# Performance work log

Hardware: AMD Instinct MI355X
Metric: run time of the kernel (lower is better)

The kernel has to match this reference:

```python
import jax, jax.numpy as jnp
import numpy as np

N = 100000
D = 128
H = 128
E = 3200000

def setup_inputs() -> dict:
    key = jax.random.key(0)
    ks = jax.random.split(key, 6)
    x = jax.random.normal(ks[0], (N, D), dtype=jnp.float32)
    edge_src = jax.random.randint(ks[1], (E,), 0, N, dtype=jnp.int32)
    edge_dst = jax.random.randint(ks[2], (E,), 0, N, dtype=jnp.int32)
    edge_w = jax.random.uniform(ks[3], (E,), dtype=jnp.float32)
    # Linear params (torch default-ish scale)
    W1 = jax.random.normal(ks[4], (D, H), dtype=jnp.float32) / np.sqrt(D)
    b1 = jnp.zeros((H,), dtype=jnp.float32)
    W2 = jax.random.normal(ks[5], (H, H), dtype=jnp.float32) / np.sqrt(H)
    b2 = jnp.zeros((H,), dtype=jnp.float32)
    return {"x": x, "edge_src": edge_src, "edge_dst": edge_dst, "edge_w": edge_w,
            "W1": W1, "b1": b1, "W2": W2, "b2": b2}

def reference(x, edge_src, edge_dst, edge_w, W1, b1, W2, b2):
    # out = spmm(A, x): weighted aggregation of source-node features at dst
    msgs = x[edge_src] * edge_w[:, None]           # [E, D]
    agg = jax.ops.segment_sum(msgs, edge_dst, num_segments=N)  # [N, D]
    out = agg + x                                   # residual
    out = jax.nn.selu(out @ W1 + b1)                # layer 1
    out = jax.nn.selu(out @ W2 + b2)                # layer 2
    return out
```

## Files before the change

### kernel.cpp

```cpp
#include <hip/hip_runtime.h>
#include <hip/hip_bf16.h>

#define SELU_LAM   1.0507009873554805f
#define SELU_ALPHA 1.6732632423543772f

#define NBSH 6
#define NPB  64
#define RCAP 4096
#define SCHUNK 16384
#define MROWS 64

typedef __attribute__((ext_vector_type(8))) short bf16x8;
typedef __attribute__((ext_vector_type(4))) float f32x4;

__device__ __forceinline__ float selu_f(float v) {
    return v > 0.0f ? SELU_LAM * v
                    : (SELU_LAM * SELU_ALPHA) * (expf(v) - 1.0f);
}

__device__ __forceinline__ unsigned bf16r(float f) {
    unsigned u = __float_as_uint(f);
    return (u + 0x7FFFu + ((u >> 16) & 1u)) >> 16;
}

__global__ __launch_bounds__(256) void prep_kernel(const float* __restrict__ x,
                                                   uint* __restrict__ xb, int nxb,
                                                   const float* __restrict__ W1,
                                                   const float* __restrict__ W2,
                                                   uint* __restrict__ wt1,
                                                   uint* __restrict__ wt2,
                                                   const int* __restrict__ edst,
                                                   int* __restrict__ bcnt, int E, int B) {
    __shared__ int lc[2048];
    for (int i = threadIdx.x; i < B; i += 256) lc[i] = 0;

    int tid = blockIdx.x * 256 + threadIdx.x;
    int stride = gridDim.x * 256;

    for (int i = tid; i < nxb; i += stride) {
        float2 v = ((const float2*)x)[i];
        xb[i] = bf16r(v.x) | (bf16r(v.y) << 16);
    }
    for (int i = tid; i < 128 * 64; i += stride) {
        int n = i & 127, kp = i >> 7;
        uint idx = (uint)(((n * 128 + 2 * kp) ^ ((n & 7) << 3)) >> 1);
        uint lo = bf16r(W1[(2 * kp) * 128 + n]);
        uint hi = bf16r(W1[(2 * kp + 1) * 128 + n]);
        wt1[idx] = lo | (hi << 16);
        lo = bf16r(W2[(2 * kp) * 128 + n]);
        hi = bf16r(W2[(2 * kp + 1) * 128 + n]);
        wt2[idx] = lo | (hi << 16);
    }
    __syncthreads();
    int n4 = E >> 2;
    for (int j = tid; j < n4; j += stride) {
        int4 d = ((const int4*)edst)[j];
        atomicAdd(&lc[d.x >> NBSH], 1);
        atomicAdd(&lc[d.y >> NBSH], 1);
        atomicAdd(&lc[d.z >> NBSH], 1);
        atomicAdd(&lc[d.w >> NBSH], 1);
    }
    for (int j = (n4 << 2) + tid; j < E; j += stride) atomicAdd(&lc[edst[j] >> NBSH], 1);
    __syncthreads();
    for (int i = threadIdx.x; i < B; i += 256) if (lc[i]) atomicAdd(&bcnt[i], lc[i]);
}

__global__ __launch_bounds__(1024) void bucket_scan(const int* __restrict__ bcnt,
                                                    int* __restrict__ boff,
                                                    int* __restrict__ bfill, int B, int E) {
    __shared__ int buf[1024];
    int t = threadIdx.x;
    int a = (2 * t     < B) ? bcnt[2 * t]     : 0;
    int b = (2 * t + 1 < B) ? bcnt[2 * t + 1] : 0;
    buf[t] = a + b; __syncthreads();
    for (int d = 1; d < 1024; d <<= 1) {
        int v = (t >= d) ? buf[t - d] : 0; __syncthreads();
        buf[t] += v; __syncthreads();
    }
    int excl = (t == 0) ? 0 : buf[t - 1];
    if (2 * t     < B) { boff[2 * t]     = excl;     bfill[2 * t]     = excl; }
    if (2 * t + 1 < B) { boff[2 * t + 1] = excl + a; bfill[2 * t + 1] = excl + a; }
    if (t == 0) boff[B] = E;
}

__global__ __launch_bounds__(1024) void chunk_scatter(const int* __restrict__ esrc,
                                                      const int* __restrict__ edst,
                                                      const float* __restrict__ ew,
                                                      int* __restrict__ bfill,
                                                      int2* __restrict__ binned,
                                                      int E, int B) {
    __shared__ int cnt[2048];
    __shared__ int base[2048];
    int tid = threadIdx.x;
    int nchunks = (E + SCHUNK - 1) / SCHUNK;

    for (int c = blockIdx.x; c < nchunks; c += gridDim.x) {
        int lo = c * SCHUNK;
        int hi = min(lo + SCHUNK, E);
        int full = lo + ((hi - lo) & ~3);

        for (int i = tid; i < B; i += 1024) cnt[i] = 0;
        __syncthreads();

        for (int i = lo + tid * 4; i < full; i += 4096) {
            int4 d = *(const int4*)(edst + i);
            atomicAdd(&cnt[d.x >> NBSH], 1);
            atomicAdd(&cnt[d.y >> NBSH], 1);
            atomicAdd(&cnt[d.z >> NBSH], 1);
            atomicAdd(&cnt[d.w >> NBSH], 1);
        }
        for (int i = full + tid; i < hi; i += 1024) atomicAdd(&cnt[edst[i] >> NBSH], 1);
        __syncthreads();

        for (int i = tid; i < B; i += 1024) {
            int c0 = cnt[i];
            base[i] = c0 ? atomicAdd(&bfill[i], c0) : 0;
            cnt[i] = 0;
        }
        __syncthreads();

        for (int i = lo + tid * 4; i < full; i += 4096) {
            int4   s = *(const int4*)(esrc + i);
            int4   d = *(const int4*)(edst + i);
            float4 w = *(const float4*)(ew + i);
            int b0 = d.x >> NBSH, b1 = d.y >> NBSH, b2 = d.z >> NBSH, b3 = d.w >> NBSH;
            int p;
            p = base[b0] + atomicAdd(&cnt[b0], 1);
            binned[p] = make_int2(s.x | ((d.x & (NPB - 1)) << 17), __float_as_int(w.x));
            p = base[b1] + atomicAdd(&cnt[b1], 1);
            binned[p] = make_int2(s.y | ((d.y & (NPB - 1)) << 17), __float_as_int(w.y));
            p = base[b2] + atomicAdd(&cnt[b2], 1);
            binned[p] = make_int2(s.z | ((d.z & (NPB - 1)) << 17), __float_as_int(w.z));
            p = base[b3] + atomicAdd(&cnt[b3], 1);
            binned[p] = make_int2(s.w | ((d.w & (NPB - 1)) << 17), __float_as_int(w.w));
        }
        for (int i = full + tid; i < hi; i += 1024) {
            int dd = edst[i];
            int b = dd >> NBSH;
            int p = base[b] + atomicAdd(&cnt[b], 1);
            binned[p] = make_int2(esrc[i] | ((dd & (NPB - 1)) << 17), __float_as_int(ew[i]));
        }
        __syncthreads();
    }
}

template<int GMODE>
__global__ __launch_bounds__(512) void sorted_gather(const uint* __restrict__ xb,
                                                     const float* __restrict__ x,
                                                     const int* __restrict__ boff,
                                                     const int2* __restrict__ binned,
                                                     float* __restrict__ out,
                                                     uint* __restrict__ hb, int N) {
    __shared__ int2 stage[RCAP];
    __shared__ int  cnt[NPB];
    __shared__ int  pref[NPB + 1];
    __shared__ int  fill[NPB];

    int b = blockIdx.x;
    int node0 = b << NBSH;
    int beg = boff[b], end = boff[b + 1];
    int count = end - beg;
    int tid = threadIdx.x;

    if (tid < NPB) cnt[tid] = 0;
    __syncthreads();

    bool sorted = (count <= RCAP);
    if (sorted) {
        for (int i = tid; i < count; i += 512)
            atomicAdd(&cnt[(binned[beg + i].x >> 17) & (NPB - 1)], 1);
        __syncthreads();
        if (tid == 0) {
            int run = 0;
            for (int k = 0; k < NPB; ++k) { pref[k] = run; run += cnt[k]; }
            pref[NPB] = run;
        }
        __syncthreads();
        if (tid < NPB) fill[tid] = pref[tid];
        __syncthreads();
        for (int i = tid; i < count; i += 512) {
            int2 d = binned[beg + i];
            int p = atomicAdd(&fill[(d.x >> 17) & (NPB - 1)], 1);
            stage[p] = d;
        }
        __syncthreads();
    }

    int wid  = tid >> 6;
    int lane = tid & 63;

    #pragma unroll 1
    for (int t = 0; t < 8; ++t) {
        int dl = wid * 8 + t;
        int node = node0 + dl;
        if (node >= N) break;

        float a0, a1;
        if (GMODE >= 1) {
            uint pr = xb[(size_t)node * 64 + lane];
            a0 = __uint_as_float(pr << 16);
            a1 = __uint_as_float(pr & 0xFFFF0000u);
        } else {
            float2 v = ((const float2*)(x + (size_t)node * 128))[lane];
            a0 = v.x; a1 = v.y;
        }

        if (sorted) {
            int e  = pref[dl];
            int e1 = pref[dl + 1];
            for (; e + 7 < e1; e += 8) {
                int2 dsc[8];
                #pragma unroll
                for (int u = 0; u < 8; ++u) dsc[u] = stage[e + u];
                if (GMODE >= 1) {
                    uint pk[8];
                    #pragma unroll
                    for (int u = 0; u < 8; ++u)
                        pk[u] = xb[(size_t)(dsc[u].x & 0x1FFFF) * 64 + lane];
                    #pragma unroll
                    for (int u = 0; u < 8; ++u) {
                        float w = __int_as_float(dsc[u].y);
                        a0 = fmaf(__uint_as_float(pk[u] << 16), w, a0);
                        a1 = fmaf(__uint_as_float(pk[u] & 0xFFFF0000u), w, a1);
                    }
                } else {
                    float2 v[8];
                    #pragma unroll
                    for (int u = 0; u < 8; ++u)
                        v[u] = ((const float2*)(x + (size_t)(dsc[u].x & 0x1FFFF) * 128))[lane];
                    #pragma unroll
                    for (int u = 0; u < 8; ++u) {
                        float w = __int_as_float(dsc[u].y);
                        a0 = fmaf(v[u].x, w, a0); a1 = fmaf(v[u].y, w, a1);
                    }
                }
            }
            for (; e < e1; ++e) {
                int2 d0 = stage[e];
                float w = __int_as_float(d0.y);
                if (GMODE >= 1) {
                    uint p0 = xb[(size_t)(d0.x & 0x1FFFF) * 64 + lane];
                    a0 = fmaf(__uint_as_float(p0 << 16), w, a0);
                    a1 = fmaf(__uint_as_float(p0 & 0xFFFF0000u), w, a1);
                } else {
                    float2 v = ((const float2*)(x + (size_t)(d0.x & 0x1FFFF) * 128))[lane];
                    a0 = fmaf(v.x, w, a0); a1 = fmaf(v.y, w, a1);
                }
            }
        } else {
            for (int e = beg; e < end; ++e) {
                int2 d0 = binned[e];
                float w = (((d0.x >> 17) & (NPB - 1)) == dl) ? __int_as_float(d0.y) : 0.0f;
                if (GMODE >= 1) {
                    uint p0 = xb[(size_t)(d0.x & 0x1FFFF) * 64 + lane];
                    a0 = fmaf(__uint_as_float(p0 << 16), w, a0);
                    a1 = fmaf(__uint_as_float(p0 & 0xFFFF0000u), w, a1);
                } else {
                    float2 v = ((const float2*)(x + (size_t)(d0.x & 0x1FFFF) * 128))[lane];
                    a0 = fmaf(v.x, w, a0); a1 = fmaf(v.y, w, a1);
                }
            }
        }

        if (GMODE == 2) {
            uint val = bf16r(a0) | (bf16r(a1) << 16);
            uint idx = (uint)((dl * 64 + lane) ^ ((dl & 7) << 2));
            hb[(size_t)b * 4096 + idx] = val;
        } else {
            ((float2*)out)[(size_t)node * 64 + lane] = make_float2(a0, a1);
        }
    }
}


__global__ __launch_bounds__(256) void copy_kernel(const float4* __restrict__ src,
                                                   float4* __restrict__ dst, int n4) {
    int i = blockIdx.x * 256 + threadIdx.x;
    if (i < n4) dst[i] = src[i];
}

__global__ __launch_bounds__(256) void scatter_kernel(const float* __restrict__ x,
                                                      const int* __restrict__ esrc,
                                                      const int* __restrict__ edst,
                                                      const float* __restrict__ ew,
                                                      float* __restrict__ agg, int E) {
    int e = blockIdx.x * 8 + (threadIdx.x >> 5);
    if (e >= E) return;
    int lane = threadIdx.x & 31;
    int s = esrc[e];
    int d = edst[e];
    float w = ew[e];
    float4 v = ((const float4*)(x + (size_t)s * 128))[lane];
    float* dp = agg + (size_t)d * 128 + lane * 4;
    atomicAdd(dp + 0, v.x * w);
    atomicAdd(dp + 1, v.y * w);
    atomicAdd(dp + 2, v.z * w);
    atomicAdd(dp + 3, v.w * w);
}

template<bool HB>
__global__ __launch_bounds__(256) void mlp_fused(const float* __restrict__ h,
                                                 const uint* __restrict__ hb,
                                                 const uint* __restrict__ wt1,
                                                 const float* __restrict__ b1,
                                                 const uint* __restrict__ wt2,
                                                 const float* __restrict__ b2,
                                                 float* __restrict__ outp, int nrows) {
    __shared__ unsigned short sW1[128 * 128];
    __shared__ unsigned short sW2[128 * 128];
    __shared__ unsigned short sH[MROWS * 128];

    int tid  = threadIdx.x;
    int row0 = blockIdx.x * MROWS;

    for (int i = tid; i < 2048; i += 256) {
        ((uint4*)sW1)[i] = ((const uint4*)wt1)[i];
        ((uint4*)sW2)[i] = ((const uint4*)wt2)[i];
    }
    if (HB) {
        for (int i = tid; i < 1024; i += 256)
            ((uint4*)sH)[i] = ((const uint4*)hb)[(size_t)blockIdx.x * 1024 + i];
    } else {
        for (int i = tid; i < MROWS * 32; i += 256) {
            int r = i >> 5, cg = i & 31;
            float4 v = (row0 + r < nrows) ? ((const float4*)h)[(size_t)(row0 + r) * 32 + cg]
                                          : make_float4(0.f, 0.f, 0.f, 0.f);
            uint p0 = bf16r(v.x) | (bf16r(v.y) << 16);
            uint p1 = bf16r(v.z) | (bf16r(v.w) << 16);
            int us = (r * 128 + cg * 4) ^ ((r & 7) << 3);
            ((uint*)sH)[us >> 1]       = p0;
            ((uint*)sH)[(us >> 1) + 1] = p1;
        }
    }
    __syncthreads();

    int lane = tid & 63;
    int wid  = tid >> 6;
    int rbase = wid * 16;
    int lr = lane & 15;
    int lq = lane >> 4;

    f32x4 acc[8];
    #pragma unroll
    for (int t = 0; t < 8; ++t) acc[t] = (f32x4){0.f, 0.f, 0.f, 0.f};

    #pragma unroll
    for (int kk = 0; kk < 4; ++kk) {
        int r = rbase + lr;
        int k = lq * 8 + kk * 32;
        bf16x8 af = *(const bf16x8*)&sH[(r * 128 + k) ^ ((r & 7) << 3)];
        #pragma unroll
        for (int t = 0; t < 8; ++t) {
            int n = t * 16 + lr;
            bf16x8 bf = *(const bf16x8*)&sW1[(n * 128 + k) ^ ((n & 7) << 3)];
            acc[t] = __builtin_amdgcn_mfma_f32_16x16x32_bf16(af, bf, acc[t], 0, 0, 0);
        }
    }
    __syncthreads();

    #pragma unroll
    for (int t = 0; t < 8; ++t) {
        int col = t * 16 + lr;
        float bv = b1[col];
        #pragma unroll
        for (int g = 0; g < 4; ++g) {
            int row = rbase + lq * 4 + g;
            float v = selu_f(acc[t][g] + bv);
            sH[(row * 128 + col) ^ ((row & 7) << 3)] = (unsigned short)bf16r(v);
        }
    }
    __syncthreads();

    #pragma unroll
    for (int t = 0; t < 8; ++t) acc[t] = (f32x4){0.f, 0.f, 0.f, 0.f};

    #pragma unroll
    for (int kk = 0; kk < 4; ++kk) {
        int r = rbase + lr;
        int k = lq * 8 + kk * 32;
        bf16x8 af = *(const bf16x8*)&sH[(r * 128 + k) ^ ((r & 7) << 3)];
        #pragma unroll
        for (int t = 0; t < 8; ++t) {
            int n = t * 16 + lr;
            bf16x8 bf = *(const bf16x8*)&sW2[(n * 128 + k) ^ ((n & 7) << 3)];
            acc[t] = __builtin_amdgcn_mfma_f32_16x16x32_bf16(af, bf, acc[t], 0, 0, 0);
        }
    }

    #pragma unroll
    for (int t = 0; t < 8; ++t) {
        int col = t * 16 + lr;
        float bv = b2[col];
        #pragma unroll
        for (int g = 0; g < 4; ++g) {
            int row = row0 + rbase + lq * 4 + g;
            if (row < nrows)
                __builtin_nontemporal_store(selu_f(acc[t][g] + bv),
                                            &outp[(size_t)row * 128 + col]);
        }
    }
}

__global__ __launch_bounds__(256) void gemm_bias_selu(const float* __restrict__ inp,
                                                      const float* __restrict__ W,
                                                      const float* __restrict__ bias,
                                                      float* __restrict__ outp, int nrows) {
    __shared__ float sW[128 * 128];
    __shared__ float sH[32 * 128];

    float4* sW4 = (float4*)sW;
    float4* sH4 = (float4*)sH;

    for (int i = threadIdx.x; i < 128 * 32; i += 256)
        sW4[i] = ((const float4*)W)[i];

    int row0 = blockIdx.x * 32;
    for (int i = threadIdx.x; i < 32 * 32; i += 256) {
        int r = row0 + (i >> 5);
        sH4[i] = (r < nrows) ? ((const float4*)inp)[(size_t)r * 32 + (i & 31)]
                             : make_float4(0.f, 0.f, 0.f, 0.f);
    }
    __syncthreads();

    int cg = threadIdx.x & 31;
    int rg = (threadIdx.x >> 5) << 2;

    float4 acc[4];
    #pragma unroll
    for (int r = 0; r < 4; ++r) acc[r] = make_float4(0.f, 0.f, 0.f, 0.f);

    #pragma unroll 4
    for (int k4 = 0; k4 < 32; ++k4) {
        float4 w0 = sW4[(k4 * 4 + 0) * 32 + cg];
        float4 w1 = sW4[(k4 * 4 + 1) * 32 + cg];
        float4 w2 = sW4[(k4 * 4 + 2) * 32 + cg];
        float4 w3 = sW4[(k4 * 4 + 3) * 32 + cg];
        #pragma unroll
        for (int r = 0; r < 4; ++r) {
            float4 h = sH4[(rg + r) * 32 + k4];
            acc[r].x = fmaf(h.x, w0.x, fmaf(h.y, w1.x, fmaf(h.z, w2.x, fmaf(h.w, w3.x, acc[r].x))));
            acc[r].y = fmaf(h.x, w0.y, fmaf(h.y, w1.y, fmaf(h.z, w2.y, fmaf(h.w, w3.y, acc[r].y))));
            acc[r].z = fmaf(h.x, w0.z, fmaf(h.y, w1.z, fmaf(h.z, w2.z, fmaf(h.w, w3.z, acc[r].z))));
            acc[r].w = fmaf(h.x, w0.w, fmaf(h.y, w1.w, fmaf(h.z, w2.w, fmaf(h.w, w3.w, acc[r].w))));
        }
    }

    float4 bv = ((const float4*)bias)[cg];
    #pragma unroll
    for (int r = 0; r < 4; ++r) {
        int row = row0 + rg + r;
        if (row < nrows) {
            float4 o;
            o.x = selu_f(acc[r].x + bv.x);
            o.y = selu_f(acc[r].y + bv.y);
            o.z = selu_f(acc[r].z + bv.z);
            o.w = selu_f(acc[r].w + bv.w);
            ((float4*)outp)[(size_t)row * 32 + cg] = o;
        }
    }
}


extern "C" void kernel_launch(void* const* d_in, const int* in_sizes, int n_in,
                              void* d_out, int out_size, void* d_ws, size_t ws_size,
                              hipStream_t stream) {
    (void)n_in; (void)out_size;
    const float* x    = (const float*)d_in[0];
    const int*   esrc = (const int*)  d_in[1];
    const int*   edst = (const int*)  d_in[2];
    const float* ew   = (const float*)d_in[3];
    const float* W1   = (const float*)d_in[4];
    const float* b1   = (const float*)d_in[5];
    const float* W2   = (const float*)d_in[6];
    const float* b2   = (const float*)d_in[7];
    float* out = (float*)d_out;

    int N = in_sizes[0] / 128;
    int E = in_sizes[1];
    int B = (N + NPB - 1) >> NBSH;
    int nb64 = (N + 63) / 64;

    size_t hdr   = ((size_t)(3 * B + 1) * 4 + 15) & ~(size_t)15;
    size_t wt_b  = 65536;
    size_t xb_b  = (size_t)N * 256;
    size_t hb_b  = (size_t)nb64 * 16384;
    size_t bin_b = (size_t)E * 8;
    size_t need_full = hdr + wt_b + xb_b + hb_b + bin_b;
    size_t need_bf16 = hdr + wt_b + xb_b + bin_b;
    size_t need_f32  = hdr + wt_b + bin_b;

    int gmode = (ws_size >= need_full) ? 2 : (ws_size >= need_bf16) ? 1
              : (ws_size >= need_f32) ? 0 : -1;
    bool use_csr = (B <= 2048) && (gmode >= 0) && (N <= 131072);

    if (use_csr) {
        int*  bcnt    = (int*)d_ws;
        int*  boff    = bcnt + B;
        int*  bfill   = boff + B + 1;
        uint* wt1     = (uint*)((char*)d_ws + hdr);
        uint* wt2     = wt1 + 8192;
        uint* xb      = (uint*)((char*)d_ws + hdr + wt_b);
        uint* hb      = (uint*)((char*)d_ws + hdr + wt_b + xb_b);
        size_t bin_off = hdr + wt_b + (gmode >= 1 ? xb_b : 0) + (gmode == 2 ? hb_b : 0);
        int2* binned  = (int2*)((char*)d_ws + bin_off);

        hipMemsetAsync(bcnt, 0, (size_t)B * 4, stream);

        prep_kernel<<<512, 256, 0, stream>>>(x, xb, gmode >= 1 ? N * 64 : 0,
                                             W1, W2, wt1, wt2, edst, bcnt, E, B);
        bucket_scan<<<1, 1024, 0, stream>>>(bcnt, boff, bfill, B, E);

        int nchunks = (E + SCHUNK - 1) / SCHUNK; if (nchunks > 2048) nchunks = 2048;
        chunk_scatter<<<nchunks, 1024, 0, stream>>>(esrc, edst, ew, bfill, binned, E, B);

        if (gmode == 2)
            sorted_gather<2><<<B, 512, 0, stream>>>(xb, x, boff, binned, out, hb, N);
        else if (gmode == 1)
            sorted_gather<1><<<B, 512, 0, stream>>>(xb, x, boff, binned, out, hb, N);
        else
            sorted_gather<0><<<B, 512, 0, stream>>>(xb, x, boff, binned, out, hb, N);

        if (gmode == 2)
            mlp_fused<true><<<nb64, 256, 0, stream>>>(out, hb, wt1, b1, wt2, b2, out, N);
        else
            mlp_fused<false><<<nb64, 256, 0, stream>>>(out, hb, wt1, b1, wt2, b2, out, N);
    } else {
        int n4 = N * 32;
        copy_kernel<<<(n4 + 255) / 256, 256, 0, stream>>>((const float4*)x, (float4*)out, n4);
        scatter_kernel<<<(E + 7) / 8, 256, 0, stream>>>(x, esrc, edst, ew, out, E);
        int gblocks = (N + 31) / 32;
        gemm_bias_selu<<<gblocks, 256, 0, stream>>>(out, W1, b1, out, N);
        gemm_bias_selu<<<gblocks, 256, 0, stream>>>(out, W2, b2, out, N);
    }
}
```

Before: 296.5 us.

## Stage bucket edges once in LDS, sort via index array, limit histogram blocks

The gather kernel now reads each bucket's binned edges from global memory once into LDS, counts them with per-wave histograms to reduce atomic contention, and sorts by writing 16-bit indices instead of moving the edge records. Edge reads in the accumulation loop go through the index array. The prep kernel limits the edge-destination histogram to the first 160 blocks so the other blocks only do conversion work. RCAP is reduced to fit the extra LDS, which sends more buckets to the slow unsorted path, and every edge read now costs an extra indirect LDS load.

```diff
diff --git a/kernel.cpp b/kernel.cpp
--- a/kernel.cpp
+++ b/kernel.cpp
@@ -6,9 +6,10 @@
 
 #define NBSH 6
 #define NPB  64
-#define RCAP 4096
-#define SCHUNK 16384
+#define RCAP 3584
+#define SCHUNK 12288
 #define MROWS 64
+#define HISTB 160
 
 typedef __attribute__((ext_vector_type(8))) short bf16x8;
 typedef __attribute__((ext_vector_type(4))) float f32x4;
@@ -32,7 +33,9 @@
                                                    const int* __restrict__ edst,
                                                    int* __restrict__ bcnt, int E, int B) {
     __shared__ int lc[2048];
-    for (int i = threadIdx.x; i < B; i += 256) lc[i] = 0;
+    bool hist = (blockIdx.x < HISTB);
+    if (hist)
+        for (int i = threadIdx.x; i < B; i += 256) lc[i] = 0;
 
     int tid = blockIdx.x * 256 + threadIdx.x;
     int stride = gridDim.x * 256;
@@ -51,18 +54,22 @@
         hi = bf16r(W2[(2 * kp + 1) * 128 + n]);
         wt2[idx] = lo | (hi << 16);
     }
-    __syncthreads();
-    int n4 = E >> 2;
-    for (int j = tid; j < n4; j += stride) {
-        int4 d = ((const int4*)edst)[j];
-        atomicAdd(&lc[d.x >> NBSH], 1);
-        atomicAdd(&lc[d.y >> NBSH], 1);
-        atomicAdd(&lc[d.z >> NBSH], 1);
-        atomicAdd(&lc[d.w >> NBSH], 1);
-    }
-    for (int j = (n4 << 2) + tid; j < E; j += stride) atomicAdd(&lc[edst[j] >> NBSH], 1);
-    __syncthreads();
-    for (int i = threadIdx.x; i < B; i += 256) if (lc[i]) atomicAdd(&bcnt[i], lc[i]);
+    if (hist) {
+        __syncthreads();
+        int htid = blockIdx.x * 256 + threadIdx.x;
+        int hstride = HISTB * 256;
+        int n4 = E >> 2;
+        for (int j = htid; j < n4; j += hstride) {
+            int4 d = ((const int4*)edst)[j];
+            atomicAdd(&lc[d.x >> NBSH], 1);
+            atomicAdd(&lc[d.y >> NBSH], 1);
+            atomicAdd(&lc[d.z >> NBSH], 1);
+            atomicAdd(&lc[d.w >> NBSH], 1);
+        }
+        for (int j = (n4 << 2) + htid; j < E; j += hstride) atomicAdd(&lc[edst[j] >> NBSH], 1);
+        __syncthreads();
+        for (int i = threadIdx.x; i < B; i += 256) if (lc[i]) atomicAdd(&bcnt[i], lc[i]);
+    }
 }
 
 __global__ __launch_bounds__(1024) void bucket_scan(const int* __restrict__ bcnt,
@@ -152,42 +159,52 @@
                                                      float* __restrict__ out,
                                                      uint* __restrict__ hb, int N) {
     __shared__ int2 stage[RCAP];
-    __shared__ int  cnt[NPB];
-    __shared__ int  pref[NPB + 1];
-    __shared__ int  fill[NPB];
+    __shared__ unsigned short sidx[RCAP];
+    __shared__ int cnt8[8][NPB];
+    __shared__ int pref[NPB + 1];
+    __shared__ int fill[NPB];
 
     int b = blockIdx.x;
     int node0 = b << NBSH;
     int beg = boff[b], end = boff[b + 1];
     int count = end - beg;
     int tid = threadIdx.x;
-
-    if (tid < NPB) cnt[tid] = 0;
+    int wid  = tid >> 6;
+    int lane = tid & 63;
+
+    for (int i = tid; i < 8 * NPB; i += 512) ((int*)cnt8)[i] = 0;
     __syncthreads();
 
     bool sorted = (count <= RCAP);
     if (sorted) {
-        for (int i = tid; i < count; i += 512)
-            atomicAdd(&cnt[(binned[beg + i].x >> 17) & (NPB - 1)], 1);
+        for (int i = tid; i < count; i += 512) {
+            int2 d = binned[beg + i];
+            stage[i] = d;
+            atomicAdd(&cnt8[wid][(d.x >> 17) & (NPB - 1)], 1);
+        }
+        __syncthreads();
+        if (tid < NPB) {
+            int s = 0;
+            #pragma unroll
+            for (int w = 0; w < 8; ++w) s += cnt8[w][tid];
+            fill[tid] = s;
+        }
         __syncthreads();
         if (tid == 0) {
             int run = 0;
-            for (int k = 0; k < NPB; ++k) { pref[k] = run; run += cnt[k]; }
+            for (int k = 0; k < NPB; ++k) { pref[k] = run; run += fill[k]; }
             pref[NPB] = run;
         }
         __syncthreads();
         if (tid < NPB) fill[tid] = pref[tid];
         __syncthreads();
         for (int i = tid; i < count; i += 512) {
-            int2 d = binned[beg + i];
+            int2 d = stage[i];
             int p = atomicAdd(&fill[(d.x >> 17) & (NPB - 1)], 1);
-            stage[p] = d;
-        }
-        __syncthreads();
-    }
-
-    int wid  = tid >> 6;
-    int lane = tid & 63;
+            sidx[p] = (unsigned short)i;
+        }
+        __syncthreads();
+    }
 
     #pragma unroll 1
     for (int t = 0; t < 8; ++t) {
@@ -211,7 +228,7 @@
             for (; e + 7 < e1; e += 8) {
                 int2 dsc[8];
                 #pragma unroll
-                for (int u = 0; u < 8; ++u) dsc[u] = stage[e + u];
+                for (int u = 0; u < 8; ++u) dsc[u] = stage[sidx[e + u]];
                 if (GMODE >= 1) {
                     uint pk[8];
                     #pragma unroll
@@ -236,7 +253,7 @@
                 }
             }
             for (; e < e1; ++e) {
-                int2 d0 = stage[e];
+                int2 d0 = stage[sidx[e]];
                 float w = __int_as_float(d0.y);
                 if (GMODE >= 1) {
                     uint p0 = xb[(size_t)(d0.x & 0x1FFFF) * 64 + lane];
```

Result: slower. 307.3 us (+3.6%).
